# Performance work log

Measured on AMD Instinct MI355X. Metric: run time of the kernel, lower is better.

Reference implementation:

```python
import jax, jax.numpy as jnp
import numpy as np
from jax import lax

P = 8; E = 192; D_MODEL = E + 4; D_STATE = 16; D_CONV = 4; EXPAND = 2
D_INNER = EXPAND * D_MODEL  # 392
DT_RANK = -(-D_MODEL // 16)  # 13
MAX_FREQ = 32


def silu(v):
    return v * jax.nn.sigmoid(v)


def layernorm(v, g, b, eps=1e-5):
    m = v.mean(-1, keepdims=True)
    var = v.var(-1, keepdims=True)
    return (v - m) / jnp.sqrt(var + eps) * g + b


def mamba(x, in_w, conv_w, conv_b, xp_w, dt_w, dt_b, A_log, Dp, out_w):
    # Standard mamba_ssm Mamba block. x: (B, L, d_model)
    B, L, _ = x.shape
    xz = x @ in_w.T                      # (B,L,2*d_inner)
    xi, z = jnp.split(xz, 2, axis=-1)
    # depthwise causal conv1d (torch pads d_conv-1 both sides then truncates to L)
    xc = jnp.transpose(xi, (0, 2, 1))    # (B,d_inner,L)
    xc = lax.conv_general_dilated(xc, conv_w[:, None, :], (1,), [(D_CONV - 1, 0)],
                                  dimension_numbers=('NCH', 'OIH', 'NCH'),
                                  feature_group_count=D_INNER)
    xc = silu(jnp.transpose(xc, (0, 2, 1)) + conv_b)  # (B,L,d_inner)
    x_dbl = xc @ xp_w.T                  # (B,L,dt_rank+2*d_state)
    dt = x_dbl[..., :DT_RANK]
    Bm = x_dbl[..., DT_RANK:DT_RANK + D_STATE]
    Cm = x_dbl[..., DT_RANK + D_STATE:]
    delta = jax.nn.softplus(dt @ dt_w.T + dt_b)       # (B,L,d_inner)
    A = -jnp.exp(A_log)                               # (d_inner,d_state)
    deltaA = jnp.exp(delta[..., None] * A)            # (B,L,d_inner,d_state)
    deltaBu = delta[..., None] * Bm[:, :, None, :] * xc[..., None]

    def step(h, inp):
        dA, dBu, c = inp
        h = dA * h + dBu
        return h, jnp.einsum('bdn,bn->bd', h, c)

    h0 = jnp.zeros((B, D_INNER, D_STATE), x.dtype)
    _, ys = lax.scan(step, h0, (deltaA.transpose(1, 0, 2, 3),
                                deltaBu.transpose(1, 0, 2, 3),
                                Cm.transpose(1, 0, 2)))
    y = ys.transpose(1, 0, 2) + Dp * xc
    y = y * silu(z)
    return y @ out_w.T


def _mk_mamba_params(key):
    ks = jax.random.split(key, 6)
    s = 0.05
    return dict(
        in_w=jax.random.normal(ks[0], (2 * D_INNER, D_MODEL)) * s,
        conv_w=jax.random.normal(ks[1], (D_INNER, D_CONV)) * s,
        conv_b=jnp.zeros((D_INNER,)),
        xp_w=jax.random.normal(ks[2], (DT_RANK + 2 * D_STATE, D_INNER)) * s,
        dt_w=jax.random.normal(ks[3], (D_INNER, DT_RANK)) * s,
        dt_b=jax.random.normal(ks[4], (D_INNER,)) * 0.1,
        A_log=jnp.log(jnp.broadcast_to(jnp.arange(1, D_STATE + 1, dtype=jnp.float32), (D_INNER, D_STATE)) + 0.0),
        D=jnp.ones((D_INNER,)),
        out_w=jax.random.normal(ks[5], (D_MODEL, D_INNER)) * s,
    )


def setup_inputs() -> dict:
    key = jax.random.key(0)
    k = jax.random.split(key, 8)
    inp = {
        'x': jax.random.normal(k[0], (16, 3, 256, 256), dtype=jnp.float32),
        'patch_w': jax.random.normal(k[1], (E, 3, P, P)) * 0.05,
        'patch_b': jnp.zeros((E,)),
        'pe_ln_g': jnp.ones((E,)), 'pe_ln_b': jnp.zeros((E,)),
        'blk_ln_g': jnp.ones((D_MODEL,)), 'blk_ln_b': jnp.zeros((D_MODEL,)),
        'cls_w': jax.random.normal(k[2], (1, D_MODEL)) * 0.05,
        'cls_b': jnp.zeros((1,)),
    }
    for pref, kk in (('f_', k[3]), ('b_', k[4])):
        for name, val in _mk_mamba_params(kk).items():
            inp[pref + name] = val
    return inp


def reference(x, patch_w, patch_b, pe_ln_g, pe_ln_b,
              f_in_w, f_conv_w, f_conv_b, f_xp_w, f_dt_w, f_dt_b, f_A_log, f_D, f_out_w,
              b_in_w, b_conv_w, b_conv_b, b_xp_w, b_dt_w, b_dt_b, b_A_log, b_D, b_out_w,
              blk_ln_g, blk_ln_b, cls_w, cls_b):
    B, C, H, W = x.shape
    hp, wp = H // P, W // P
    # PatchEmbed: stride==kernel conv expressed as one GEMM over patches
    xp = x.reshape(B, C, hp, P, wp, P)
    tok = jnp.einsum('bchpwq,ecpq->bhwe', xp, patch_w) + patch_b
    tok = tok.reshape(B, hp * wp, E)
    tok = silu(layernorm(tok, pe_ln_g, pe_ln_b))
    # RotaryEmbedding: concat 4 positional channels
    L = hp * wp
    scale = 2 * np.pi / MAX_FREQ
    pos = jnp.arange(L, dtype=tok.dtype)[:, None] * scale
    row = (jnp.arange(L) // MAX_FREQ).astype(tok.dtype)[:, None] * scale
    cp = jnp.concatenate([jnp.sin(pos), jnp.cos(pos), jnp.sin(row), jnp.cos(row)], axis=-1)
    h = jnp.concatenate([tok, jnp.broadcast_to(cp[None], (B, L, 4))], axis=-1)  # (B,L,196)
    # BidirectionalMambaBlock
    fo = mamba(h, f_in_w, f_conv_w, f_conv_b, f_xp_w, f_dt_w, f_dt_b, f_A_log, f_D, f_out_w)
    bo = jnp.flip(mamba(jnp.flip(h, 1), b_in_w, b_conv_w, b_conv_b, b_xp_w, b_dt_w, b_dt_b, b_A_log, b_D, b_out_w), 1)
    out = (fo + bo) * 0.5
    out = silu(layernorm(out, blk_ln_g, blk_ln_b)) + h
    # Classifier: mean pool + linear (num_classes==2 -> 1 logit)
    return out.mean(1) @ cls_w.T + cls_b
```

## Files before the change

### kernel.cpp

```cpp
#include <hip/hip_runtime.h>
#include <cstdint>
#include <cstddef>

constexpr int B_   = 16;
constexpr int L_   = 1024;
constexpr int E_   = 192;
constexpr int DM   = 196;
constexpr int DI   = 392;
constexpr int DS   = 16;
constexpr int DTR  = 13;
constexpr int NTOK = B_ * L_;
constexpr int XDW  = DTR + 2 * DS;
constexpr int CH   = B_ * DI;

constexpr int KP_XZ = 224;
constexpr int KP_OP = 416;
constexpr int KP_PW = 192;

constexpr size_t HW_SZ = (size_t)NTOK * DM;
constexpr size_t DI_SZ = (size_t)NTOK * DI;

constexpr size_t O_H     = 0;
constexpr size_t O_H16   = 3211264;
constexpr size_t O_XI_F  = 5046272;
constexpr size_t O_XI_B  = 11468800;
constexpr size_t O_Z_F   = 17891328;
constexpr size_t O_Z_B   = 24313856;
constexpr size_t O_XC_F  = 30736384;
constexpr size_t O_XC_B  = 37158912;
constexpr size_t O_DTR_F = 43581440;
constexpr size_t O_DTR_B = 43794432;
constexpr size_t O_BC_F  = 44007424;
constexpr size_t O_BC_B  = 44531712;
constexpr size_t O_YS_F  = 45056000;
constexpr size_t O_YS_B  = 48267264;
constexpr size_t O_PW16  = 51478528;
constexpr size_t O_FIN16 = 51496960;
constexpr size_t O_BIN16 = 51584768;
constexpr size_t O_FOUT16= 51672576;
constexpr size_t O_BOUT16= 51713344;

typedef _Float16 half8 __attribute__((ext_vector_type(8)));
typedef float f32x4v __attribute__((ext_vector_type(4)));

__device__ __forceinline__ float siluf(float x) {
    return x / (1.f + __expf(-x));
}

__device__ __forceinline__ float blk_sum(float v, float* red) {
    #pragma unroll
    for (int o = 32; o > 0; o >>= 1) v += __shfl_down(v, o);
    int w = threadIdx.x >> 6;
    __syncthreads();
    if ((threadIdx.x & 63) == 0) red[w] = v;
    __syncthreads();
    return red[0] + red[1] + red[2] + red[3];
}

__global__ __launch_bounds__(256) void cvt_all(const float* __restrict__ pw,
                                               const float* __restrict__ fin,
                                               const float* __restrict__ bin,
                                               const float* __restrict__ fout,
                                               const float* __restrict__ bout,
                                               _Float16* __restrict__ dst) {
    int i = blockIdx.x * 256 + threadIdx.x;
    const float* src; int K, Kp, off;
    if (i < 36864)       { src = pw;   K = 192; Kp = 192; off = i; }
    else if (i < 212480) { src = fin;  K = 196; Kp = 224; off = i - 36864; }
    else if (i < 388096) { src = bin;  K = 196; Kp = 224; off = i - 212480; }
    else if (i < 469632) { src = fout; K = 392; Kp = 416; off = i - 388096; }
    else                 { src = bout; K = 392; Kp = 416; off = i - 469632; }
    int n = off / Kp, k = off - n * Kp;
    dst[i] = (_Float16)(k < K ? src[(size_t)n * K + k] : 0.f);
}

__global__ __launch_bounds__(256) void gather_patch(const float* __restrict__ x,
                                                    _Float16* __restrict__ Xp) {
    int i = blockIdx.x * 256 + threadIdx.x;
    int tok = i / 192, r = i - tok * 192;
    int c = r >> 6, pq = r & 63, p = pq >> 3, q = pq & 7;
    int b = tok >> 10, l = tok & 1023, hh = l >> 5, wv = l & 31;
    Xp[i] = (_Float16)x[(((size_t)(b * 3 + c) * 256 + hh * 8 + p) << 8) + wv * 8 + q];
}

template <int MODE>
__device__ __forceinline__ void mfma_core(const _Float16* __restrict__ A,
                                          const _Float16* __restrict__ W,
                                          const float* __restrict__ bias,
                                          float* __restrict__ C,
                                          int N, int Kpad, int ldc,
                                          int flip, int m_blk, int n_blk) {
    const int tid = threadIdx.x;
    const int wv = tid >> 6, lane = tid & 63;
    const int col = lane & 15, quad = lane >> 4;
    const int m_base = m_blk * 128 + wv * 32;
    const int n_base = n_blk * 64;

    int r0 = m_base + col, r1 = m_base + 16 + col;
    if (flip) {
        r0 = (r0 & ~1023) + (1023 - (r0 & 1023));
        r1 = (r1 & ~1023) + (1023 - (r1 & 1023));
    }
    const _Float16* a0p = A + (size_t)r0 * Kpad + quad * 8;
    const _Float16* a1p = A + (size_t)r1 * Kpad + quad * 8;

    const _Float16* bp[4];
    bool bok[4];
    #pragma unroll
    for (int j = 0; j < 4; ++j) {
        int n = n_base + j * 16 + col;
        bok[j] = (n < N);
        bp[j] = W + (size_t)(bok[j] ? n : 0) * Kpad + quad * 8;
    }

    f32x4v acc[2][4];
    #pragma unroll
    for (int i = 0; i < 2; ++i)
        #pragma unroll
        for (int j = 0; j < 4; ++j)
            #pragma unroll
            for (int r = 0; r < 4; ++r) acc[i][j][r] = 0.f;

    half8 bzero;
    #pragma unroll
    for (int q = 0; q < 8; ++q) bzero[q] = (_Float16)0.f;

    for (int k0 = 0; k0 < Kpad; k0 += 32) {
        half8 a0 = *(const half8*)(a0p + k0);
        half8 a1 = *(const half8*)(a1p + k0);
        #pragma unroll
        for (int j = 0; j < 4; ++j) {
            half8 bv = bzero;
            if (bok[j]) bv = *(const half8*)(bp[j] + k0);
            acc[0][j] = __builtin_amdgcn_mfma_f32_16x16x32_f16(a0, bv, acc[0][j], 0, 0, 0);
            acc[1][j] = __builtin_amdgcn_mfma_f32_16x16x32_f16(a1, bv, acc[1][j], 0, 0, 0);
        }
    }

    if (MODE == 0) {
        #pragma unroll
        for (int i = 0; i < 2; ++i) {
            int mrow = m_base + i * 16 + quad * 4;
            #pragma unroll
            for (int j = 0; j < 4; ++j) {
                int n = n_base + j * 16 + col;
                if (n < N) {
                    float bv = bias ? bias[n] : 0.f;
                    #pragma unroll
                    for (int r = 0; r < 4; ++r)
                        C[(size_t)(mrow + r) * ldc + n] = acc[i][j][r] + bv;
                }
            }
        }
    } else {
        const int bb = m_base >> 10;
        const int t0 = m_base & 1023;
        #pragma unroll
        for (int i = 0; i < 2; ++i) {
            int tt = t0 + i * 16 + quad * 4;
            #pragma unroll
            for (int j = 0; j < 4; ++j) {
                int n = n_base + j * 16 + col;
                if (n < N) {
                    float4 v = {acc[i][j][0], acc[i][j][1], acc[i][j][2], acc[i][j][3]};
                    *(float4*)(C + (((size_t)(bb * N + n)) << 10) + tt) = v;
                }
            }
        }
    }
}

__global__ __launch_bounds__(256) void mfma_patch(const _Float16* __restrict__ A,
                                                  const _Float16* __restrict__ W,
                                                  const float* __restrict__ bias,
                                                  float* __restrict__ C) {
    mfma_core<0>(A, W, bias, C, 192, KP_PW, 192, 0, blockIdx.x, blockIdx.y);
}

__global__ __launch_bounds__(256) void mfma_xz(const _Float16* __restrict__ A,
                                               const _Float16* __restrict__ Wf,
                                               const _Float16* __restrict__ Wb,
                                               float* __restrict__ C0, float* __restrict__ C1,
                                               float* __restrict__ C2, float* __restrict__ C3) {
    const int zi = blockIdx.z;
    const _Float16* W = (zi < 2 ? Wf : Wb) + (size_t)(zi & 1) * DI * KP_XZ;
    float* C = (zi == 0) ? C0 : (zi == 1) ? C1 : (zi == 2) ? C2 : C3;
    mfma_core<1>(A, W, nullptr, C, DI, KP_XZ, 0, zi >> 1, blockIdx.x, blockIdx.y);
}

__global__ __launch_bounds__(256) void mfma_op(const _Float16* __restrict__ Af,
                                               const _Float16* __restrict__ Ab,
                                               const _Float16* __restrict__ Wf,
                                               const _Float16* __restrict__ Wb,
                                               float* __restrict__ Cf, float* __restrict__ Cb) {
    const int zi = blockIdx.z;
    mfma_core<0>(zi ? Ab : Af, zi ? Wb : Wf, nullptr, zi ? Cb : Cf,
                 DM, KP_OP, DM, 0, blockIdx.x, blockIdx.y);
}

__global__ __launch_bounds__(256) void ln_silu_pos(const float* __restrict__ tok,
                                                   const float* __restrict__ g,
                                                   const float* __restrict__ bb,
                                                   float* __restrict__ h,
                                                   _Float16* __restrict__ h16) {
    const int w = threadIdx.x >> 6, lane = threadIdx.x & 63;
    const int t = blockIdx.x * 4 + w;
    const float* tp = tok + (size_t)t * E_;
    float v[3];
    float s1 = 0.f, s2 = 0.f;
    #pragma unroll
    for (int i = 0; i < 3; ++i) {
        v[i] = tp[lane + i * 64];
        s1 += v[i];
        s2 = fmaf(v[i], v[i], s2);
    }
    #pragma unroll
    for (int o = 32; o > 0; o >>= 1) {
        s1 += __shfl_xor(s1, o);
        s2 += __shfl_xor(s2, o);
    }
    float mean = s1 * (1.f / E_);
    float var = s2 * (1.f / E_) - mean * mean;
    float inv = rsqrtf(var + 1e-5f);
    float* hp = h + (size_t)t * DM;
    _Float16* hq = h16 + (size_t)t * KP_XZ;
    #pragma unroll
    for (int i = 0; i < 3; ++i) {
        int e = lane + i * 64;
        float o = siluf((v[i] - mean) * inv * g[e] + bb[e]);
        hp[e] = o;
        hq[e] = (_Float16)o;
    }
    const int l = t & 1023;
    const float scale = 0.19634954084936207f;
    if (lane < 4) {
        float pv = (lane == 0) ? sinf(l * scale)
                 : (lane == 1) ? cosf(l * scale)
                 : (lane == 2) ? sinf((float)(l >> 5) * scale)
                 :               cosf((float)(l >> 5) * scale);
        hp[E_ + lane] = pv;
        hq[E_ + lane] = (_Float16)pv;
    } else if (lane < 32) {
        hq[192 + lane] = (_Float16)0.f;
    }
}

__global__ __launch_bounds__(256) void conv_silu_T(
        const float* __restrict__ xiT_f, const float* __restrict__ xiT_b,
        float* __restrict__ xcT_f, float* __restrict__ xcT_b,
        const float* __restrict__ fw, const float* __restrict__ fb,
        const float* __restrict__ bw, const float* __restrict__ bb2) {
    int i = blockIdx.x * 256 + threadIdx.x;
    int rall = i >> 8;
    int dir = rall >= CH;
    int r = rall - (dir ? CH : 0);
    int d = r % DI;
    int t0 = (i & 255) << 2;
    const float* xi = (dir ? xiT_b : xiT_f) + ((size_t)r << 10) + t0;
    float cur[4], prev[4] = {0.f, 0.f, 0.f, 0.f};
    *(float4*)cur = *(const float4*)xi;
    if (t0) *(float4*)prev = *(const float4*)(xi - 4);
    const float* w = (dir ? bw : fw) + d * 4;
    float bias = (dir ? bb2 : fb)[d];
    float xv[7] = {prev[1], prev[2], prev[3], cur[0], cur[1], cur[2], cur[3]};
    float o[4];
    #pragma unroll
    for (int tt = 0; tt < 4; ++tt) {
        float a = bias;
        #pragma unroll
        for (int k = 0; k < 4; ++k) a = fmaf(xv[tt + k], w[k], a);
        o[tt] = siluf(a);
    }
    *(float4*)((dir ? xcT_b : xcT_f) + ((size_t)r << 10) + t0) = *(float4*)o;
}

__global__ __launch_bounds__(256) void gemm_xdbl(const float* __restrict__ Af,
                                                 const float* __restrict__ Ab,
                                                 const float* __restrict__ Wf,
                                                 const float* __restrict__ Wb,
                                                 float* __restrict__ dtrf,
                                                 float* __restrict__ dtrb,
                                                 float* __restrict__ bcf,
                                                 float* __restrict__ bcb) {
    const int yi = blockIdx.y;
    const float* A = yi ? Ab : Af;
    const float* W = yi ? Wb : Wf;
    float* dtr = yi ? dtrb : dtrf;
    float* bc = yi ? bcb : bcf;
    __shared__ __align__(16) float As[16][68];
    __shared__ __align__(16) float Ws[16][68];
    const int m0 = blockIdx.x * 64;
    const int t = threadIdx.x;
    const int tx = t & 15, ty = t >> 4;
    float acc[4][4] = {};
    const int arow_l = t >> 2;
    const int kq = (t & 3) * 4;
    const int bb_ = m0 >> 10, tt0 = m0 & 1023;
    for (int kt = 0; kt < 25; ++kt) {
        const int k0 = kt << 4;
        {
            int kr = t >> 4, tc = t & 15;
            int kk = k0 + kr;
            float4 v = {0.f, 0.f, 0.f, 0.f};
            if (kk < DI)
                v = *(const float4*)(A + (((size_t)bb_ * DI + kk) << 10) + tt0 + tc * 4);
            *(float4*)&As[kr][tc * 4] = v;
        }
        {
            bool okn = arow_l < XDW;
            const float* wp = W + (size_t)arow_l * DI;
            #pragma unroll
            for (int jj = 0; jj < 4; ++jj) {
                int kk = k0 + kq + jj;
                Ws[kq + jj][arow_l] = (okn && kk < DI) ? wp[kk] : 0.f;
            }
        }
        __syncthreads();
        #pragma unroll
        for (int k = 0; k < 16; ++k) {
            float av[4], wv[4];
            *(float4*)av = *(const float4*)&As[k][ty * 4];
            *(float4*)wv = *(const float4*)&Ws[k][tx * 4];
            #pragma unroll
            for (int i = 0; i < 4; ++i)
                #pragma unroll
                for (int j = 0; j < 4; ++j)
                    acc[i][j] = fmaf(av[i], wv[j], acc[i][j]);
        }
        __syncthreads();
    }
    #pragma unroll
    for (int i = 0; i < 4; ++i) {
        int m = m0 + ty * 4 + i;
        #pragma unroll
        for (int j = 0; j < 4; ++j) {
            int n = tx * 4 + j;
            float v = acc[i][j];
            if (n < DTR) dtr[(size_t)m * DTR + n] = v;
            else if (n < XDW) bc[(size_t)m * 32 + (n - DTR)] = v;
        }
    }
}

__global__ __launch_bounds__(256) void delta_kernel(
        const float* __restrict__ dtr_f, const float* __restrict__ dtr_b,
        float* __restrict__ dlT_f, float* __restrict__ dlT_b,
        const float* __restrict__ f_dt_w, const float* __restrict__ f_dt_b,
        const float* __restrict__ b_dt_w, const float* __restrict__ b_dt_b) {
    int i = blockIdx.x * 256 + threadIdx.x;
    int dir = i >= (int)DI_SZ;
    int j = dir ? i - (int)DI_SZ : i;
    int r = j >> 10, t = j & 1023;
    int b = r / DI, d = r - (r / DI) * DI;
    size_t tok = ((size_t)b << 10) + t;
    const float* xd = (dir ? dtr_b : dtr_f) + tok * DTR;
    const float* w = (dir ? b_dt_w : f_dt_w) + d * DTR;
    float acc = (dir ? b_dt_b : f_dt_b)[d];
    #pragma unroll
    for (int q = 0; q < DTR; ++q) acc = fmaf(xd[q], w[q], acc);
    float sp = fmaxf(acc, 0.f) + log1pf(__expf(-fabsf(acc)));
    (dir ? dlT_b : dlT_f)[j] = sp;
}

__global__ __launch_bounds__(256) void scan_kernel(
        const float* __restrict__ dlT_f, const float* __restrict__ dlT_b,
        const float* __restrict__ xcT_f, const float* __restrict__ xcT_b,
        const float* __restrict__ bc_f,  const float* __restrict__ bc_b,
        const float* __restrict__ zT_f,  const float* __restrict__ zT_b,
        _Float16* __restrict__ y16_f,    _Float16* __restrict__ y16_b,
        const float* __restrict__ fA, const float* __restrict__ bA,
        const float* __restrict__ fD, const float* __restrict__ bD) {
    __shared__ float sP[8][8][16];
    __shared__ float sH[8][8][16];
    __shared__ float sI[8][8][16];
    const int tid = threadIdx.x;
    const int ni = tid & 3;
    const int c  = (tid >> 2) & 7;
    const int ch_l = tid >> 5;
    const int chain = blockIdx.x * 8 + ch_l;
    const int dir = chain >= CH;
    const int r = chain - (dir ? CH : 0);
    const int b = r / DI, d = r - (r / DI) * DI;

    const float* dlT = (dir ? dlT_b : dlT_f) + ((size_t)r << 10);
    const float* uT  = (dir ? xcT_b : xcT_f) + ((size_t)r << 10);
    const float* zT  = (dir ? zT_b  : zT_f)  + ((size_t)r << 10);
    const float* BC  = (dir ? bc_b  : bc_f)  + (((size_t)b << 10) * 32);
    _Float16* y16    = (dir ? y16_b : y16_f) + ((size_t)r << 10);
    const float* Al  = (dir ? bA : fA) + d * DS + ni * 4;
    float Av[4];
    #pragma unroll
    for (int i = 0; i < 4; ++i) Av[i] = -__expf(Al[i]);
    const float Dd = (dir ? bD : fD)[d];
    const int t0 = c << 7;

    if (c < 7) {
        float h[4] = {0.f, 0.f, 0.f, 0.f};
        float S = 0.f;
        for (int g = 0; g < 32; ++g) {
            const int tg = t0 + g * 4;
            float4 d4 = *(const float4*)(dlT + tg);
            float4 u4 = *(const float4*)(uT + tg);
            float dv[4] = {d4.x, d4.y, d4.z, d4.w};
            float uv[4] = {u4.x, u4.y, u4.z, u4.w};
            #pragma unroll
            for (int tt = 0; tt < 4; ++tt) {
                float4 B4 = *(const float4*)(BC + (size_t)(tg + tt) * 32 + ni * 4);
                float w = dv[tt] * uv[tt];
                S += dv[tt];
                float Bv[4] = {B4.x, B4.y, B4.z, B4.w};
                #pragma unroll
                for (int i = 0; i < 4; ++i)
                    h[i] = fmaf(__expf(dv[tt] * Av[i]), h[i], w * Bv[i]);
            }
        }
        #pragma unroll
        for (int i = 0; i < 4; ++i) {
            sP[ch_l][c][ni * 4 + i] = __expf(S * Av[i]);
            sH[ch_l][c][ni * 4 + i] = h[i];
        }
    }
    __syncthreads();

    if (tid < 128) {
        const int ch = tid >> 4, n = tid & 15;
        float hi = 0.f;
        #pragma unroll
        for (int cc = 0; cc < 8; ++cc) {
            sI[ch][cc][n] = hi;
            if (cc < 7) hi = sH[ch][cc][n] + sP[ch][cc][n] * hi;
        }
    }
    __syncthreads();

    {
        float h[4];
        #pragma unroll
        for (int i = 0; i < 4; ++i) h[i] = sI[ch_l][c][ni * 4 + i];
        _Float16 ybuf[8] __attribute__((aligned(16)));
        for (int g = 0; g < 32; ++g) {
            const int tg = t0 + g * 4;
            float4 d4 = *(const float4*)(dlT + tg);
            float4 u4 = *(const float4*)(uT + tg);
            float4 z4 = *(const float4*)(zT + tg);
            float dv[4] = {d4.x, d4.y, d4.z, d4.w};
            float uv[4] = {u4.x, u4.y, u4.z, u4.w};
            float zv[4] = {z4.x, z4.y, z4.z, z4.w};
            float pq[4];
            #pragma unroll
            for (int tt = 0; tt < 4; ++tt) {
                float4 B4 = *(const float4*)(BC + (size_t)(tg + tt) * 32 + ni * 4);
                float4 C4 = *(const float4*)(BC + (size_t)(tg + tt) * 32 + 16 + ni * 4);
                float w = dv[tt] * uv[tt];
                float Bv[4] = {B4.x, B4.y, B4.z, B4.w};
                float Cv[4] = {C4.x, C4.y, C4.z, C4.w};
                float p = 0.f;
                #pragma unroll
                for (int i = 0; i < 4; ++i) {
                    h[i] = fmaf(__expf(dv[tt] * Av[i]), h[i], w * Bv[i]);
                    p = fmaf(h[i], Cv[i], p);
                }
                pq[tt] = p;
            }
            #pragma unroll
            for (int tt = 0; tt < 4; ++tt) {
                pq[tt] += __shfl_xor(pq[tt], 1);
                pq[tt] += __shfl_xor(pq[tt], 2);
            }
            if (((g >> 1) & 3) == ni) {
                const int base = (g & 1) * 4;
                #pragma unroll
                for (int tt = 0; tt < 4; ++tt)
                    ybuf[base + tt] =
                        (_Float16)((pq[tt] + Dd * uv[tt]) * siluf(zv[tt]));
            }
            if ((g & 7) == 7)
                *(half8*)(y16 + t0 + ((g >> 3) << 5) + ni * 8) = *(half8*)ybuf;
        }
    }
}

__global__ __launch_bounds__(256) void transp_y(
        const _Float16* __restrict__ yf, const _Float16* __restrict__ yb,
        _Float16* __restrict__ of, _Float16* __restrict__ ob) {
    __shared__ _Float16 tile[64][72];
    const int dblk = blockIdx.z % 7, dir = blockIdx.z / 7;
    const int b = blockIdx.y, tb = blockIdx.x;
    const _Float16* y = dir ? yb : yf;
    _Float16* o = dir ? ob : of;
    const int d0 = dblk * 64, t0 = tb * 64;
    const int dl = threadIdx.x >> 2, ts = (threadIdx.x & 3) * 16;
    const int d = d0 + dl;
    if (d < DI) {
        const _Float16* src = y + (((size_t)(b * DI + d)) << 10) + t0 + ts;
        *(half8*)&tile[dl][ts] = *(const half8*)src;
        *(half8*)&tile[dl][ts + 8] = *(const half8*)(src + 8);
    } else {
        #pragma unroll
        for (int q = 0; q < 16; ++q) tile[dl][ts + q] = (_Float16)0.f;
    }
    __syncthreads();
    const int tl = threadIdx.x >> 2, ds = (threadIdx.x & 3) * 16;
    if (d0 + ds < KP_OP) {
        _Float16 v[16] __attribute__((aligned(16)));
        #pragma unroll
        for (int q = 0; q < 16; ++q) v[q] = tile[ds + q][tl];
        _Float16* dst = o + ((size_t)((b << 10) + t0 + tl)) * KP_OP + d0 + ds;
        *(half8*)dst = *(half8*)&v[0];
        *(half8*)(dst + 8) = *(half8*)&v[8];
    }
}

__global__ __launch_bounds__(256) void final_head(
        const float* __restrict__ fo, const float* __restrict__ bo,
        const float* __restrict__ h, const float* __restrict__ g,
        const float* __restrict__ bb, const float* __restrict__ cls_w,
        float* __restrict__ partial) {
    const int w = threadIdx.x >> 6, lane = threadIdx.x & 63;
    const int t = blockIdx.x * 4 + w;
    const int b = t >> 10, l = t & 1023;
    const float* fp = fo + (size_t)t * DM;
    const float* bp = bo + ((size_t)(b << 10) + (1023 - l)) * DM;
    const float* hp = h + (size_t)t * DM;
    float v[4];
    float s1 = 0.f, s2 = 0.f;
    #pragma unroll
    for (int i = 0; i < 4; ++i) {
        int e = lane + i * 64;
        bool ok = (i < 3) || (lane < 4);
        float vv = ok ? 0.5f * (fp[e] + bp[e]) : 0.f;
        v[i] = vv;
        s1 += vv;
        s2 = fmaf(vv, vv, s2);
    }
    #pragma unroll
    for (int o = 32; o > 0; o >>= 1) {
        s1 += __shfl_xor(s1, o);
        s2 += __shfl_xor(s2, o);
    }
    float mean = s1 * (1.f / DM);
    float var = s2 * (1.f / DM) - mean * mean;
    float inv = rsqrtf(var + 1e-5f);
    float c = 0.f;
    #pragma unroll
    for (int i = 0; i < 4; ++i) {
        int e = lane + i * 64;
        bool ok = (i < 3) || (lane < 4);
        if (ok) {
            float o2 = (v[i] - mean) * inv * g[e] + bb[e];
            o2 = siluf(o2) + hp[e];
            c = fmaf(o2, cls_w[e], c);
        }
    }
    #pragma unroll
    for (int o = 32; o > 0; o >>= 1) c += __shfl_xor(c, o);
    if (lane == 0) partial[t] = c;
}

__global__ __launch_bounds__(256) void head_reduce(const float* __restrict__ partial,
                                                   const float* __restrict__ cls_b,
                                                   float* __restrict__ out) {
    __shared__ float red[4];
    const int b = blockIdx.x;
    const float* p = partial + ((size_t)b << 10);
    float s = 0.f;
    for (int i = threadIdx.x; i < 1024; i += 256) s += p[i];
    s = blk_sum(s, red);
    if (threadIdx.x == 0) out[b] = s * (1.f / 1024.f) + cls_b[0];
}

extern "C" void kernel_launch(void* const* d_in, const int* in_sizes, int n_in,
                              void* d_out, int out_size, void* d_ws, size_t ws_size,
                              hipStream_t stream) {
    const float* x        = (const float*)d_in[0];
    const float* patch_w  = (const float*)d_in[1];
    const float* patch_b  = (const float*)d_in[2];
    const float* pe_g     = (const float*)d_in[3];
    const float* pe_b     = (const float*)d_in[4];
    const float* blk_g    = (const float*)d_in[5];
    const float* blk_b    = (const float*)d_in[6];
    const float* cls_w    = (const float*)d_in[7];
    const float* cls_b    = (const float*)d_in[8];
    const float* f_in_w   = (const float*)d_in[9];
    const float* f_conv_w = (const float*)d_in[10];
    const float* f_conv_b = (const float*)d_in[11];
    const float* f_xp_w   = (const float*)d_in[12];
    const float* f_dt_w   = (const float*)d_in[13];
    const float* f_dt_b   = (const float*)d_in[14];
    const float* f_A_log  = (const float*)d_in[15];
    const float* f_D      = (const float*)d_in[16];
    const float* f_out_w  = (const float*)d_in[17];
    const float* b_in_w   = (const float*)d_in[18];
    const float* b_conv_w = (const float*)d_in[19];
    const float* b_conv_b = (const float*)d_in[20];
    const float* b_xp_w   = (const float*)d_in[21];
    const float* b_dt_w   = (const float*)d_in[22];
    const float* b_dt_b   = (const float*)d_in[23];
    const float* b_A_log  = (const float*)d_in[24];
    const float* b_D      = (const float*)d_in[25];
    const float* b_out_w  = (const float*)d_in[26];

    float* ws = (float*)d_ws;
    float* out = (float*)d_out;

    float* Hb        = ws + O_H;
    _Float16* H16    = (_Float16*)(ws + O_H16);
    float* XIf       = ws + O_XI_F;
    float* XIb       = ws + O_XI_B;
    float* Zf        = ws + O_Z_F;
    float* Zb        = ws + O_Z_B;
    _Float16* YsTf16 = (_Float16*)(ws + O_Z_F);
    _Float16* YsTb16 = (_Float16*)(ws + O_Z_B);
    float* XCf       = ws + O_XC_F;
    float* XCb       = ws + O_XC_B;
    float* DTRf      = ws + O_DTR_F;
    float* DTRb      = ws + O_DTR_B;
    float* BCf       = ws + O_BC_F;
    float* BCb       = ws + O_BC_B;
    _Float16* Xp16   = (_Float16*)(ws + O_YS_F);
    float* TokRaw    = ws + O_YS_B;
    _Float16* Y16f   = (_Float16*)(ws + O_YS_F);
    _Float16* Y16b   = (_Float16*)(ws + O_YS_B);
    _Float16* PW16   = (_Float16*)(ws + O_PW16);
    _Float16* FIN16  = (_Float16*)(ws + O_FIN16);
    _Float16* BIN16  = (_Float16*)(ws + O_BIN16);
    _Float16* FOUT16 = (_Float16*)(ws + O_FOUT16);
    _Float16* BOUT16 = (_Float16*)(ws + O_BOUT16);

    cvt_all<<<2153, 256, 0, stream>>>(patch_w, f_in_w, b_in_w, f_out_w, b_out_w, PW16);

    gather_patch<<<(NTOK * 192) / 256, 256, 0, stream>>>(x, Xp16);
    mfma_patch<<<dim3(NTOK / 128, 3), 256, 0, stream>>>(Xp16, PW16, patch_b, TokRaw);
    ln_silu_pos<<<NTOK / 4, 256, 0, stream>>>(TokRaw, pe_g, pe_b, Hb, H16);

    mfma_xz<<<dim3(NTOK / 128, 7, 4), 256, 0, stream>>>(H16, FIN16, BIN16,
                                                        XIf, Zf, XIb, Zb);
    conv_silu_T<<<2 * CH, 256, 0, stream>>>(XIf, XIb, XCf, XCb,
                                            f_conv_w, f_conv_b, b_conv_w, b_conv_b);
    gemm_xdbl<<<dim3(NTOK / 64, 2), 256, 0, stream>>>(XCf, XCb, f_xp_w, b_xp_w,
                                                      DTRf, DTRb, BCf, BCb);
    delta_kernel<<<(2 * (int)DI_SZ) / 256, 256, 0, stream>>>(
        DTRf, DTRb, XIf, XIb, f_dt_w, f_dt_b, b_dt_w, b_dt_b);
    scan_kernel<<<2 * CH / 8, 256, 0, stream>>>(
        XIf, XIb, XCf, XCb, BCf, BCb, Zf, Zb, Y16f, Y16b,
        f_A_log, b_A_log, f_D, b_D);
    transp_y<<<dim3(16, 16, 14), 256, 0, stream>>>(Y16f, Y16b, YsTf16, YsTb16);
    mfma_op<<<dim3(NTOK / 128, 4, 2), 256, 0, stream>>>(YsTf16, YsTb16,
                                                        FOUT16, BOUT16, XIf, XIb);
    final_head<<<NTOK / 4, 256, 0, stream>>>(XIf, XIb, Hb, blk_g, blk_b, cls_w, XCf);
    head_reduce<<<B_, 256, 0, stream>>>(XCf, cls_b, out);
}
```

Measured before the change: 518.9 us.

## Replace chunked two-pass scan with serial per-state scan and transposed B/C

Replaces the chunked two-pass selective scan, which split each chain into 8 time chunks and fixed them up through shared memory, with a single serial pass. In the new pass each of 16 lanes owns one state element and the outputs are reduced with xor shuffles. gemm_xdbl now writes B and C time-major per (batch, state) through a shared-memory transpose, so the scan reads them as contiguous float4 streams with one-step-ahead prefetch. The z half of the input projection is stored as fp16 to cut bandwidth. In exchange, the serial dependency length per chain goes from 128 to 1024 steps and each step adds four shuffle rounds, trading parallelism for fewer reads and no second pass.

```diff
diff --git a/kernel.cpp b/kernel.cpp
--- a/kernel.cpp
+++ b/kernel.cpp
@@ -41,6 +41,7 @@
 constexpr size_t O_BOUT16= 51713344;
 
 typedef _Float16 half8 __attribute__((ext_vector_type(8)));
+typedef _Float16 half4v __attribute__((ext_vector_type(4)));
 typedef float f32x4v __attribute__((ext_vector_type(4)));
 
 __device__ __forceinline__ float siluf(float x) {
@@ -87,7 +88,7 @@
 __device__ __forceinline__ void mfma_core(const _Float16* __restrict__ A,
                                           const _Float16* __restrict__ W,
                                           const float* __restrict__ bias,
-                                          float* __restrict__ C,
+                                          void* __restrict__ Cv_,
                                           int N, int Kpad, int ldc,
                                           int flip, int m_blk, int n_blk) {
     const int tid = threadIdx.x;
@@ -138,6 +139,7 @@
     }
 
     if (MODE == 0) {
+        float* C = (float*)Cv_;
         #pragma unroll
         for (int i = 0; i < 2; ++i) {
             int mrow = m_base + i * 16 + quad * 4;
@@ -162,8 +164,15 @@
             for (int j = 0; j < 4; ++j) {
                 int n = n_base + j * 16 + col;
                 if (n < N) {
-                    float4 v = {acc[i][j][0], acc[i][j][1], acc[i][j][2], acc[i][j][3]};
-                    *(float4*)(C + (((size_t)(bb * N + n)) << 10) + tt) = v;
+                    if (MODE == 1) {
+                        float4 v = {acc[i][j][0], acc[i][j][1], acc[i][j][2], acc[i][j][3]};
+                        *(float4*)((float*)Cv_ + (((size_t)(bb * N + n)) << 10) + tt) = v;
+                    } else {
+                        half4v v;
+                        #pragma unroll
+                        for (int r = 0; r < 4; ++r) v[r] = (_Float16)acc[i][j][r];
+                        *(half4v*)((_Float16*)Cv_ + (((size_t)(bb * N + n)) << 10) + tt) = v;
+                    }
                 }
             }
         }
@@ -180,12 +189,15 @@
 __global__ __launch_bounds__(256) void mfma_xz(const _Float16* __restrict__ A,
                                                const _Float16* __restrict__ Wf,
                                                const _Float16* __restrict__ Wb,
-                                               float* __restrict__ C0, float* __restrict__ C1,
-                                               float* __restrict__ C2, float* __restrict__ C3) {
+                                               float* __restrict__ C0, _Float16* __restrict__ C1,
+                                               float* __restrict__ C2, _Float16* __restrict__ C3) {
     const int zi = blockIdx.z;
     const _Float16* W = (zi < 2 ? Wf : Wb) + (size_t)(zi & 1) * DI * KP_XZ;
-    float* C = (zi == 0) ? C0 : (zi == 1) ? C1 : (zi == 2) ? C2 : C3;
-    mfma_core<1>(A, W, nullptr, C, DI, KP_XZ, 0, zi >> 1, blockIdx.x, blockIdx.y);
+    const int flip = zi >> 1;
+    if (zi == 0)      mfma_core<1>(A, W, nullptr, C0, DI, KP_XZ, 0, flip, blockIdx.x, blockIdx.y);
+    else if (zi == 1) mfma_core<2>(A, W, nullptr, C1, DI, KP_XZ, 0, flip, blockIdx.x, blockIdx.y);
+    else if (zi == 2) mfma_core<1>(A, W, nullptr, C2, DI, KP_XZ, 0, flip, blockIdx.x, blockIdx.y);
+    else              mfma_core<2>(A, W, nullptr, C3, DI, KP_XZ, 0, flip, blockIdx.x, blockIdx.y);
 }
 
 __global__ __launch_bounds__(256) void mfma_op(const _Float16* __restrict__ Af,
@@ -289,6 +301,7 @@
     float* bc = yi ? bcb : bcf;
     __shared__ __align__(16) float As[16][68];
     __shared__ __align__(16) float Ws[16][68];
+    __shared__ __align__(16) float Ls[32][68];
     const int m0 = blockIdx.x * 64;
     const int t = threadIdx.x;
     const int tx = t & 15, ty = t >> 4;
@@ -337,8 +350,18 @@
             int n = tx * 4 + j;
             float v = acc[i][j];
             if (n < DTR) dtr[(size_t)m * DTR + n] = v;
-            else if (n < XDW) bc[(size_t)m * 32 + (n - DTR)] = v;
-        }
+            else if (n < XDW) Ls[n - DTR][ty * 4 + i] = v;
+        }
+    }
+    __syncthreads();
+    {
+        int nn = t >> 3;
+        int tq = (t & 7) * 8;
+        float4 v0 = *(const float4*)&Ls[nn][tq];
+        float4 v1 = *(const float4*)&Ls[nn][tq + 4];
+        float* dst = bc + (((size_t)(bb_ * 32 + nn)) << 10) + tt0 + tq;
+        *(float4*)dst = v0;
+        *(float4*)(dst + 4) = v1;
     }
 }
 
@@ -362,121 +385,73 @@
     (dir ? dlT_b : dlT_f)[j] = sp;
 }
 
-__global__ __launch_bounds__(256) void scan_kernel(
+__global__ __launch_bounds__(256) void scan_serial(
         const float* __restrict__ dlT_f, const float* __restrict__ dlT_b,
         const float* __restrict__ xcT_f, const float* __restrict__ xcT_b,
-        const float* __restrict__ bc_f,  const float* __restrict__ bc_b,
-        const float* __restrict__ zT_f,  const float* __restrict__ zT_b,
+        const float* __restrict__ bct_f, const float* __restrict__ bct_b,
+        const _Float16* __restrict__ zT_f, const _Float16* __restrict__ zT_b,
         _Float16* __restrict__ y16_f,    _Float16* __restrict__ y16_b,
         const float* __restrict__ fA, const float* __restrict__ bA,
         const float* __restrict__ fD, const float* __restrict__ bD) {
-    __shared__ float sP[8][8][16];
-    __shared__ float sH[8][8][16];
-    __shared__ float sI[8][8][16];
     const int tid = threadIdx.x;
-    const int ni = tid & 3;
-    const int c  = (tid >> 2) & 7;
-    const int ch_l = tid >> 5;
-    const int chain = blockIdx.x * 8 + ch_l;
+    const int n = tid & 15, ch_l = tid >> 4;
+    const int chain = blockIdx.x * 16 + ch_l;
     const int dir = chain >= CH;
     const int r = chain - (dir ? CH : 0);
     const int b = r / DI, d = r - (r / DI) * DI;
 
-    const float* dlT = (dir ? dlT_b : dlT_f) + ((size_t)r << 10);
-    const float* uT  = (dir ? xcT_b : xcT_f) + ((size_t)r << 10);
-    const float* zT  = (dir ? zT_b  : zT_f)  + ((size_t)r << 10);
-    const float* BC  = (dir ? bc_b  : bc_f)  + (((size_t)b << 10) * 32);
-    _Float16* y16    = (dir ? y16_b : y16_f) + ((size_t)r << 10);
-    const float* Al  = (dir ? bA : fA) + d * DS + ni * 4;
-    float Av[4];
-    #pragma unroll
-    for (int i = 0; i < 4; ++i) Av[i] = -__expf(Al[i]);
+    const float* dl = (dir ? dlT_b : dlT_f) + ((size_t)r << 10);
+    const float* uT = (dir ? xcT_b : xcT_f) + ((size_t)r << 10);
+    const _Float16* zT = (dir ? zT_b : zT_f) + ((size_t)r << 10);
+    const float* Bp = (dir ? bct_b : bct_f) + (((size_t)(b * 32 + n)) << 10);
+    const float* Cp = Bp + (16 << 10);
+    _Float16* y16 = (dir ? y16_b : y16_f) + ((size_t)r << 10);
+    const float Av = -__expf((dir ? bA : fA)[d * DS + n]);
     const float Dd = (dir ? bD : fD)[d];
-    const int t0 = c << 7;
-
-    if (c < 7) {
-        float h[4] = {0.f, 0.f, 0.f, 0.f};
-        float S = 0.f;
-        for (int g = 0; g < 32; ++g) {
-            const int tg = t0 + g * 4;
-            float4 d4 = *(const float4*)(dlT + tg);
-            float4 u4 = *(const float4*)(uT + tg);
-            float dv[4] = {d4.x, d4.y, d4.z, d4.w};
-            float uv[4] = {u4.x, u4.y, u4.z, u4.w};
+
+    float h = 0.f;
+    _Float16 ybuf[8] __attribute__((aligned(16)));
+
+    float4 d4 = *(const float4*)dl;
+    float4 u4 = *(const float4*)uT;
+    float4 B4 = *(const float4*)Bp;
+    float4 C4 = *(const float4*)Cp;
+    half4v z4 = *(const half4v*)zT;
+
+    for (int g = 0; g < 256; ++g) {
+        const int gn = (g < 255) ? (g + 1) * 4 : 255 * 4;
+        float4 d4n = *(const float4*)(dl + gn);
+        float4 u4n = *(const float4*)(uT + gn);
+        float4 B4n = *(const float4*)(Bp + gn);
+        float4 C4n = *(const float4*)(Cp + gn);
+        half4v z4n = *(const half4v*)(zT + gn);
+
+        float dv[4] = {d4.x, d4.y, d4.z, d4.w};
+        float uv[4] = {u4.x, u4.y, u4.z, u4.w};
+        float Bv[4] = {B4.x, B4.y, B4.z, B4.w};
+        float Cv[4] = {C4.x, C4.y, C4.z, C4.w};
+        float pq[4];
+        #pragma unroll
+        for (int tt = 0; tt < 4; ++tt) {
+            float dA = __expf(dv[tt] * Av);
+            h = fmaf(dA, h, dv[tt] * uv[tt] * Bv[tt]);
+            float p = h * Cv[tt];
+            p += __shfl_xor(p, 1);
+            p += __shfl_xor(p, 2);
+            p += __shfl_xor(p, 4);
+            p += __shfl_xor(p, 8);
+            pq[tt] = p;
+        }
+        if (((g >> 1) & 15) == n) {
+            const int base = (g & 1) * 4;
             #pragma unroll
-            for (int tt = 0; tt < 4; ++tt) {
-                float4 B4 = *(const float4*)(BC + (size_t)(tg + tt) * 32 + ni * 4);
-                float w = dv[tt] * uv[tt];
-                S += dv[tt];
-                float Bv[4] = {B4.x, B4.y, B4.z, B4.w};
-                #pragma unroll
-                for (int i = 0; i < 4; ++i)
-                    h[i] = fmaf(__expf(dv[tt] * Av[i]), h[i], w * Bv[i]);
-            }
-        }
-        #pragma unroll
-        for (int i = 0; i < 4; ++i) {
-            sP[ch_l][c][ni * 4 + i] = __expf(S * Av[i]);
-            sH[ch_l][c][ni * 4 + i] = h[i];
-        }
-    }
-    __syncthreads();
-
-    if (tid < 128) {
-        const int ch = tid >> 4, n = tid & 15;
-        float hi = 0.f;
-        #pragma unroll
-        for (int cc = 0; cc < 8; ++cc) {
-            sI[ch][cc][n] = hi;
-            if (cc < 7) hi = sH[ch][cc][n] + sP[ch][cc][n] * hi;
-        }
-    }
-    __syncthreads();
-
-    {
-        float h[4];
-        #pragma unroll
-        for (int i = 0; i < 4; ++i) h[i] = sI[ch_l][c][ni * 4 + i];
-        _Float16 ybuf[8] __attribute__((aligned(16)));
-        for (int g = 0; g < 32; ++g) {
-            const int tg = t0 + g * 4;
-            float4 d4 = *(const float4*)(dlT + tg);
-            float4 u4 = *(const float4*)(uT + tg);
-            float4 z4 = *(const float4*)(zT + tg);
-            float dv[4] = {d4.x, d4.y, d4.z, d4.w};
-            float uv[4] = {u4.x, u4.y, u4.z, u4.w};
-            float zv[4] = {z4.x, z4.y, z4.z, z4.w};
-            float pq[4];
-            #pragma unroll
-            for (int tt = 0; tt < 4; ++tt) {
-                float4 B4 = *(const float4*)(BC + (size_t)(tg + tt) * 32 + ni * 4);
-                float4 C4 = *(const float4*)(BC + (size_t)(tg + tt) * 32 + 16 + ni * 4);
-                float w = dv[tt] * uv[tt];
-                float Bv[4] = {B4.x, B4.y, B4.z, B4.w};
-                float Cv[4] = {C4.x, C4.y, C4.z, C4.w};
-                float p = 0.f;
-                #pragma unroll
-                for (int i = 0; i < 4; ++i) {
-                    h[i] = fmaf(__expf(dv[tt] * Av[i]), h[i], w * Bv[i]);
-                    p = fmaf(h[i], Cv[i], p);
-                }
-                pq[tt] = p;
-            }
-            #pragma unroll
-            for (int tt = 0; tt < 4; ++tt) {
-                pq[tt] += __shfl_xor(pq[tt], 1);
-                pq[tt] += __shfl_xor(pq[tt], 2);
-            }
-            if (((g >> 1) & 3) == ni) {
-                const int base = (g & 1) * 4;
-                #pragma unroll
-                for (int tt = 0; tt < 4; ++tt)
-                    ybuf[base + tt] =
-                        (_Float16)((pq[tt] + Dd * uv[tt]) * siluf(zv[tt]));
-            }
-            if ((g & 7) == 7)
-                *(half8*)(y16 + t0 + ((g >> 3) << 5) + ni * 8) = *(half8*)ybuf;
-        }
+            for (int tt = 0; tt < 4; ++tt)
+                ybuf[base + tt] =
+                    (_Float16)((pq[tt] + Dd * uv[tt]) * siluf((float)z4[tt]));
+        }
+        if ((g & 31) == 31)
+            *(half8*)(y16 + ((g >> 5) << 7) + n * 8) = *(half8*)ybuf;
+        d4 = d4n; u4 = u4n; B4 = B4n; C4 = C4n; z4 = z4n;
     }
 }
 
@@ -607,8 +582,8 @@
     _Float16* H16    = (_Float16*)(ws + O_H16);
     float* XIf       = ws + O_XI_F;
     float* XIb       = ws + O_XI_B;
-    float* Zf        = ws + O_Z_F;
-    float* Zb        = ws + O_Z_B;
+    _Float16* ZT16f  = (_Float16*)(ws + O_Z_F);
+    _Float16* ZT16b  = (_Float16*)(ws + O_Z_B);
     _Float16* YsTf16 = (_Float16*)(ws + O_Z_F);
     _Float16* YsTb16 = (_Float16*)(ws + O_Z_B);
     float* XCf       = ws + O_XC_F;
@@ -634,15 +609,15 @@
     ln_silu_pos<<<NTOK / 4, 256, 0, stream>>>(TokRaw, pe_g, pe_b, Hb, H16);
 
     mfma_xz<<<dim3(NTOK / 128, 7, 4), 256, 0, stream>>>(H16, FIN16, BIN16,
-                                                        XIf, Zf, XIb, Zb);
+                                                        XIf, ZT16f, XIb, ZT16b);
     conv_silu_T<<<2 * CH, 256, 0, stream>>>(XIf, XIb, XCf, XCb,
                                             f_conv_w, f_conv_b, b_conv_w, b_conv_b);
     gemm_xdbl<<<dim3(NTOK / 64, 2), 256, 0, stream>>>(XCf, XCb, f_xp_w, b_xp_w,
                                                       DTRf, DTRb, BCf, BCb);
     delta_kernel<<<(2 * (int)DI_SZ) / 256, 256, 0, stream>>>(
         DTRf, DTRb, XIf, XIb, f_dt_w, f_dt_b, b_dt_w, b_dt_b);
-    scan_kernel<<<2 * CH / 8, 256, 0, stream>>>(
-        XIf, XIb, XCf, XCb, BCf, BCb, Zf, Zb, Y16f, Y16b,
+    scan_serial<<<2 * CH / 16, 256, 0, stream>>>(
+        XIf, XIb, XCf, XCb, BCf, BCb, ZT16f, ZT16b, Y16f, Y16b,
         f_A_log, b_A_log, f_D, b_D);
     transp_y<<<dim3(16, 16, 14), 256, 0, stream>>>(Y16f, Y16b, YsTf16, YsTb16);
     mfma_op<<<dim3(NTOK / 128, 4, 2), 256, 0, stream>>>(YsTf16, YsTb16,
```

Result: slower. 704.9 us (+35.9%).
